# Kernel optimization log

Hardware: AMD Instinct MI355X
Metric: run time of the kernel (lower is better)

The kernel has to match this reference:

```python
import jax, jax.numpy as jnp
import numpy as np

IMAGE_W = 256
IMAGE_H = 256
SIGMA = 0.2
EPS = 1e-07


def _gauss_filter(g, size, psize, pad):
    """g: [B,N] center coords in pixels. Returns [B,N,size,psize]."""
    # grid coords over padded canvas: value i - pad at row i (matches np.indices - pad)
    coords = jnp.arange(size + 2 * pad, dtype=jnp.float32) - pad          # [size+2pad]
    offs = jnp.arange(1, psize + 1, dtype=jnp.float32) - psize / 2 - 0.5  # [psize]
    mu = g[:, :, None] + offs[None, None, :]                              # [B,N,psize]
    F = jnp.exp(-(coords[None, None, :, None] - mu[:, :, None, :]) ** 2 / (2 * SIGMA ** 2))
    F = F / (F.sum(axis=2, keepdims=True) + EPS)
    return F[:, :, pad:size + pad]                                        # [B,N,size,psize]


def setup_inputs() -> dict:
    key = jax.random.key(0)
    k1, k2 = jax.random.split(key)
    brushes = jax.random.uniform(k1, (32, 64, 2), dtype=jnp.float32)
    patches = jax.random.normal(k2, (32, 64, 3, 16, 16), dtype=jnp.float32)
    return {"brushes": brushes, "patches": patches}


def reference(brushes, patches):
    B, N, C, ph, pw = patches.shape
    pad = ph // 2  # pad='half_patch'
    gx = brushes[:, :, 0] * IMAGE_W  # [B,N]
    gy = brushes[:, :, 1] * IMAGE_H
    Fx = _gauss_filter(gx, IMAGE_W, pw, pad)  # [B,N,w,pw]
    Fy = _gauss_filter(gy, IMAGE_H, ph, pad)  # [B,N,h,ph]
    # contract over pw: [B,N,C,w,ph]
    t = jnp.einsum('bnwq,bncpq->bncwp', Fx, patches)
    # contract over ph: [B,N,C,w,h]
    out = jnp.einsum('bncwp,bnhp->bncwh', t, Fy)
    out = out.mean(axis=1)            # [B,C,w,h]
    out = jnp.swapaxes(out, 2, 3)     # [B,C,h,w]
    return out
```

## Files before the change

kernel.cpp:

```cpp
#include <hip/hip_runtime.h>
#include <hip/hip_bf16.h>


#define TILE 16

__global__ __launch_bounds__(256) void brush_tile(
        const float* __restrict__ brushes,
        const float* __restrict__ patches,
        float* __restrict__ out)
{
    const int b   = blockIdx.z;
    const int tx  = blockIdx.x * TILE;
    const int ty  = blockIdx.y * TILE;
    const int tid = threadIdx.x;
    const int w   = tx + (tid & 15);
    const int h   = ty + (tid >> 4);

    __shared__ float  gxy[128];
    __shared__ unsigned long long smask;
    __shared__ float4 sp4[16 * 21];
    __shared__ float4 T4 [16 * 21];
    __shared__ float  invZ[32];

    if (tid < 32) {
        float4 v = ((const float4*)(brushes + (b << 7)))[tid];
        v.x *= 256.0f; v.y *= 256.0f; v.z *= 256.0f; v.w *= 256.0f;
        ((float4*)gxy)[tid] = v;
    }
    __syncthreads();

    if (tid < 64) {
        const float gx = gxy[2 * tid], gy = gxy[2 * tid + 1];
        const bool hit =
            (gx >= (float)tx - 9.5f) & (gx <= (float)tx + 24.5f) &
            (gy >= (float)ty - 9.5f) & (gy <= (float)ty + 24.5f);
        const unsigned long long m = __ballot(hit);
        if (tid == 0) smask = m;
    }
    __syncthreads();
    unsigned long long mask = smask;

    float acc0 = 0.0f, acc1 = 0.0f, acc2 = 0.0f;
    const float fh = (float)h;
    const float E25 = 1.3887944e-11f;

    while (mask) {
        const int n = __builtin_ctzll(mask);
        mask &= mask - 1;
        const float gx = gxy[2 * n], gy = gxy[2 * n + 1];

        const float* pb = patches + (size_t)((b << 6) + n) * 768;
        const float r0 = pb[tid];
        const float r1 = pb[tid + 256];
        const float r2 = pb[tid + 512];

        if (tid < 32) {
            const int axis = tid >> 4, q = tid & 15;
            const float g  = axis ? gy : gx;
            const float mu = g + (float)q - 7.5f;
            const float fl = floorf(mu);
            float Z = 0.0f;
#pragma unroll
            for (int d = -1; d <= 2; ++d) {
                const float c = fl + (float)d;
                if (c >= -8.0f && c <= 263.0f) {
                    const float u = c - mu;
                    Z += __expf(-12.5f * u * u);
                }
            }
            invZ[tid] = 1.0f / (Z + 1e-7f);
        }
        __syncthreads();

        {
            const int q = tid & 15, p = tid >> 4;
            const float zx = invZ[q];
            sp4[p * 21 + q] = make_float4(r0 * zx, r1 * zx, r2 * zx, 0.0f);
            if (tid < 64)
                sp4[(tid >> 2) * 21 + 16 + (tid & 3)] = make_float4(0, 0, 0, 0);
        }
        __syncthreads();

        {
            const int wi = tid & 15, p = tid >> 4;
            const float ax = (float)(tx + wi) - gx + 7.5f;
            float4 s = make_float4(0, 0, 0, 0);
            if (ax >= -2.5f && ax <= 17.5f) {
                int qlo = (int)ceilf(ax - 2.0f);
                qlo = qlo < 0 ? 0 : (qlo > 15 ? 15 : qlo);
                const float d0 = ax - (float)qlo;
                float wgt = __expf(-12.5f * d0 * d0);
                float u   = __expf(25.0f * d0 - 12.5f);
                const float4* row = &sp4[p * 21 + qlo];
#pragma unroll
                for (int j = 0; j < 5; ++j) {
                    const float4 v = row[j];
                    s.x += wgt * v.x; s.y += wgt * v.y; s.z += wgt * v.z;
                    wgt *= u; u *= E25;
                }
                const float zy = invZ[16 + p];
                s.x *= zy; s.y *= zy; s.z *= zy;
            }
            T4[wi * 21 + p] = s;
            if (tid < 64)
                T4[(tid >> 2) * 21 + 16 + (tid & 3)] = make_float4(0, 0, 0, 0);
        }
        __syncthreads();

        {
            const float ay = fh - gy + 7.5f;
            if (ay >= -2.5f && ay <= 17.5f) {
                int plo = (int)ceilf(ay - 2.0f);
                plo = plo < 0 ? 0 : (plo > 15 ? 15 : plo);
                const float d0 = ay - (float)plo;
                float wgt = __expf(-12.5f * d0 * d0);
                float u   = __expf(25.0f * d0 - 12.5f);
                const float4* row = &T4[(tid & 15) * 21 + plo];
#pragma unroll
                for (int j = 0; j < 5; ++j) {
                    const float4 v = row[j];
                    acc0 += wgt * v.x; acc1 += wgt * v.y; acc2 += wgt * v.z;
                    wgt *= u; u *= E25;
                }
            }
        }
    }

    const float sc = 1.0f / 64.0f;
    float* ob = out + (((size_t)(b * 3)) << 16) + (h << 8) + w;
    ob[0]       = acc0 * sc;
    ob[1 << 16] = acc1 * sc;
    ob[2 << 16] = acc2 * sc;
}

extern "C" void kernel_launch(void* const* d_in, const int* in_sizes, int n_in,
                              void* d_out, int out_size, void* d_ws, size_t ws_size,
                              hipStream_t stream) {
    const float* brushes = (const float*)d_in[0];
    const float* patches = (const float*)d_in[1];
    float* out = (float*)d_out;
    brush_tile<<<dim3(16, 16, 32), dim3(256), 0, stream>>>(brushes, patches, out);
}
```

Before: 79.40 us.

## Replace shared-memory patch staging with wavefront shuffles and drop a barrier

The first contraction now reads the normalized patch values straight from other lanes' registers with cross-lane shuffles instead of staging them through a shared float4 buffer. This removes the sp4 buffer and one block-wide barrier per brush. Brush coordinate loading is folded into the hit-test step, which saves another barrier. The T4 zero padding is now written once before the loop. The cost is 15 shuffles per brush, plus masking logic for out-of-range taps that replaces the padded shared-memory reads.

```diff
diff --git a/kernel.cpp b/kernel.cpp
--- a/kernel.cpp
+++ b/kernel.cpp
@@ -13,27 +13,26 @@
     const int tx  = blockIdx.x * TILE;
     const int ty  = blockIdx.y * TILE;
     const int tid = threadIdx.x;
-    const int w   = tx + (tid & 15);
-    const int h   = ty + (tid >> 4);
+    const int qi  = tid & 15;
+    const int pi  = tid >> 4;
+    const int w   = tx + qi;
+    const int h   = ty + pi;
 
     __shared__ float  gxy[128];
     __shared__ unsigned long long smask;
-    __shared__ float4 sp4[16 * 21];
-    __shared__ float4 T4 [16 * 21];
     __shared__ float  invZ[32];
+    __shared__ float4 T4[16 * 21];
 
-    if (tid < 32) {
-        float4 v = ((const float4*)(brushes + (b << 7)))[tid];
-        v.x *= 256.0f; v.y *= 256.0f; v.z *= 256.0f; v.w *= 256.0f;
-        ((float4*)gxy)[tid] = v;
-    }
-    __syncthreads();
+    if (tid < 80)
+        T4[(tid / 5) * 21 + 16 + (tid % 5)] = make_float4(0, 0, 0, 0);
 
     if (tid < 64) {
-        const float gx = gxy[2 * tid], gy = gxy[2 * tid + 1];
+        float2 g = ((const float2*)brushes)[(b << 6) + tid];
+        g.x *= 256.0f; g.y *= 256.0f;
+        ((float2*)gxy)[tid] = g;
         const bool hit =
-            (gx >= (float)tx - 9.5f) & (gx <= (float)tx + 24.5f) &
-            (gy >= (float)ty - 9.5f) & (gy <= (float)ty + 24.5f);
+            (g.x >= (float)tx - 9.5f) & (g.x <= (float)tx + 24.5f) &
+            (g.y >= (float)ty - 9.5f) & (g.y <= (float)ty + 24.5f);
         const unsigned long long m = __ballot(hit);
         if (tid == 0) smask = m;
     }
@@ -41,7 +40,6 @@
     unsigned long long mask = smask;
 
     float acc0 = 0.0f, acc1 = 0.0f, acc2 = 0.0f;
-    const float fh = (float)h;
     const float E25 = 1.3887944e-11f;
 
     while (mask) {
@@ -72,50 +70,44 @@
         }
         __syncthreads();
 
+        const float zx = invZ[qi];
+        const float v0 = r0 * zx, v1 = r1 * zx, v2 = r2 * zx;
+
         {
-            const int q = tid & 15, p = tid >> 4;
-            const float zx = invZ[q];
-            sp4[p * 21 + q] = make_float4(r0 * zx, r1 * zx, r2 * zx, 0.0f);
-            if (tid < 64)
-                sp4[(tid >> 2) * 21 + 16 + (tid & 3)] = make_float4(0, 0, 0, 0);
+            const float ax  = (float)w - gx + 7.5f;
+            const bool  okx = (ax >= -2.5f) & (ax <= 17.5f);
+            int qlo = (int)ceilf(ax - 2.0f);
+            qlo = qlo < 0 ? 0 : (qlo > 15 ? 15 : qlo);
+            float d0 = ax - (float)qlo;
+            d0 = fminf(fmaxf(d0, -3.0f), 3.0f);
+            float wgt = okx ? __expf(-12.5f * d0 * d0) : 0.0f;
+            float u   = __expf(25.0f * d0 - 12.5f);
+            const int base = ((pi & 3) << 4) + qlo;
+            float4 s = make_float4(0, 0, 0, 0);
+#pragma unroll
+            for (int j = 0; j < 5; ++j) {
+                const float a0 = __shfl(v0, base + j, 64);
+                const float a1 = __shfl(v1, base + j, 64);
+                const float a2 = __shfl(v2, base + j, 64);
+                const float wj = (qlo + j < 16) ? wgt : 0.0f;
+                s.x += wj * a0; s.y += wj * a1; s.z += wj * a2;
+                wgt *= u; u *= E25;
+            }
+            const float zy = invZ[16 + pi];
+            s.x *= zy; s.y *= zy; s.z *= zy;
+            T4[qi * 21 + pi] = s;
         }
         __syncthreads();
 
         {
-            const int wi = tid & 15, p = tid >> 4;
-            const float ax = (float)(tx + wi) - gx + 7.5f;
-            float4 s = make_float4(0, 0, 0, 0);
-            if (ax >= -2.5f && ax <= 17.5f) {
-                int qlo = (int)ceilf(ax - 2.0f);
-                qlo = qlo < 0 ? 0 : (qlo > 15 ? 15 : qlo);
-                const float d0 = ax - (float)qlo;
-                float wgt = __expf(-12.5f * d0 * d0);
-                float u   = __expf(25.0f * d0 - 12.5f);
-                const float4* row = &sp4[p * 21 + qlo];
-#pragma unroll
-                for (int j = 0; j < 5; ++j) {
-                    const float4 v = row[j];
-                    s.x += wgt * v.x; s.y += wgt * v.y; s.z += wgt * v.z;
-                    wgt *= u; u *= E25;
-                }
-                const float zy = invZ[16 + p];
-                s.x *= zy; s.y *= zy; s.z *= zy;
-            }
-            T4[wi * 21 + p] = s;
-            if (tid < 64)
-                T4[(tid >> 2) * 21 + 16 + (tid & 3)] = make_float4(0, 0, 0, 0);
-        }
-        __syncthreads();
-
-        {
-            const float ay = fh - gy + 7.5f;
+            const float ay = (float)h - gy + 7.5f;
             if (ay >= -2.5f && ay <= 17.5f) {
                 int plo = (int)ceilf(ay - 2.0f);
                 plo = plo < 0 ? 0 : (plo > 15 ? 15 : plo);
                 const float d0 = ay - (float)plo;
                 float wgt = __expf(-12.5f * d0 * d0);
                 float u   = __expf(25.0f * d0 - 12.5f);
-                const float4* row = &T4[(tid & 15) * 21 + plo];
+                const float4* row = &T4[qi * 21 + plo];
 #pragma unroll
                 for (int j = 0; j < 5; ++j) {
                     const float4 v = row[j];
```

Result: no change. 78.55 us (median of 2 runs) (-1.1%).
